# Kernel tuning notes

Measured on AMD Instinct MI355X. Metric: run time of the kernel, lower is better.

## Reference

```python
import jax, jax.numpy as jnp
import numpy as np

# Static config (matches init_kwargs)
VOCAB, EMBED, HIDDEN = 32000, 256, 512
SLOTS, MEM_DIM, HEADS, TOPK = 1024, 64, 4, 8
B, T = 16, 128
# beta_read/beta_write are learned scalars but the torch forward detaches them
# via .item(); treat as constants (|beta| + 1e-6 with beta init ~1.0).
BETA_R = 1.0 + 1e-6
BETA_W = 1.0 + 1e-6
EPS = 1e-8


def setup_inputs() -> dict:
    key = jax.random.key(0)
    ks = jax.random.split(key, 16)
    s = 0.02
    HD = HEADS * MEM_DIM
    return {
        "input_seq": jax.random.randint(ks[0], (B, T), 0, VOCAB),
        "E": jax.random.normal(ks[1], (VOCAB, EMBED), jnp.float32) * s,
        "W_ih": jax.random.normal(ks[2], (4 * HIDDEN, EMBED + MEM_DIM), jnp.float32) * s,
        "W_hh": jax.random.normal(ks[3], (4 * HIDDEN, HIDDEN), jnp.float32) * s,
        "b_ih": jnp.zeros((4 * HIDDEN,), jnp.float32),
        "b_hh": jnp.zeros((4 * HIDDEN,), jnp.float32),
        "W_out": jax.random.normal(ks[4], (HIDDEN, VOCAB), jnp.float32) * s,
        "b_out": jnp.zeros((VOCAB,), jnp.float32),
        "W_rk": jax.random.normal(ks[5], (HIDDEN, HD), jnp.float32) * s,
        "b_rk": jnp.zeros((HD,), jnp.float32),
        "W_wk": jax.random.normal(ks[6], (HIDDEN, HD), jnp.float32) * s,
        "b_wk": jnp.zeros((HD,), jnp.float32),
        "W_wv": jax.random.normal(ks[7], (HIDDEN, HD), jnp.float32) * s,
        "b_wv": jnp.zeros((HD,), jnp.float32),
        "W_er": jax.random.normal(ks[8], (HIDDEN, HD), jnp.float32) * s,
        "b_er": jnp.zeros((HD,), jnp.float32),
    }


def _address(memory, keys, beta):
    # memory: [B,S,D], keys: [B,H,D] -> sparse (top-k) content weights [B,H,S]
    mem_n = memory / (jnp.linalg.norm(memory, axis=-1, keepdims=True) + EPS)
    key_n = keys / (jnp.linalg.norm(keys, axis=-1, keepdims=True) + EPS)
    scores = beta * jnp.einsum("bhd,bsd->bhs", key_n, mem_n)
    vals, idx = jax.lax.top_k(scores, TOPK)           # [B,H,K]
    sm = jax.nn.softmax(vals, axis=-1)                # softmax over top-k only
    w = jnp.zeros_like(scores)
    b_ix = jnp.arange(scores.shape[0])[:, None, None]
    h_ix = jnp.arange(HEADS)[None, :, None]
    return w.at[b_ix, h_ix, idx].set(sm)              # [B,H,S]


def reference(input_seq, E, W_ih, W_hh, b_ih, b_hh, W_out, b_out,
              W_rk, b_rk, W_wk, b_wk, W_wv, b_wv, W_er, b_er):
    Bq = input_seq.shape[0]
    memory0 = jnp.full((Bq, SLOTS, MEM_DIM), 1e-6, jnp.float32)
    h0 = jnp.zeros((Bq, HIDDEN), jnp.float32)
    c0 = jnp.zeros((Bq, HIDDEN), jnp.float32)
    r0 = jnp.zeros((Bq, MEM_DIM), jnp.float32)

    def step(carry, x_t):
        memory, h, c, read_vec = carry
        emb = E[x_t]                                          # [B,embed]
        inp = jnp.concatenate([emb, read_vec], axis=-1)
        gates = inp @ W_ih.T + b_ih + h @ W_hh.T + b_hh       # [B,4H]
        i, f, g, o = jnp.split(gates, 4, axis=-1)             # torch LSTM order
        c = jax.nn.sigmoid(f) * c + jax.nn.sigmoid(i) * jnp.tanh(g)
        h = jax.nn.sigmoid(o) * jnp.tanh(c)
        logits = h @ W_out + b_out                            # [B,V]
        rk = (h @ W_rk + b_rk).reshape(Bq, HEADS, MEM_DIM)
        wk = (h @ W_wk + b_wk).reshape(Bq, HEADS, MEM_DIM)
        wv = (h @ W_wv + b_wv).reshape(Bq, HEADS, MEM_DIM)
        er = jax.nn.sigmoid(h @ W_er + b_er).reshape(Bq, HEADS, MEM_DIM)
        # content-addressed top-k read
        rw = _address(memory, rk, BETA_R)                     # [B,H,S]
        read_vec = jnp.einsum("bhs,bsd->bhd", rw, memory).mean(axis=1)
        # erase + add write
        ww = _address(memory, wk, BETA_W)                     # [B,H,S]
        keep = jnp.prod(1.0 - ww[..., None] * er[:, :, None, :], axis=1)
        add = jnp.einsum("bhs,bhd->bsd", ww, wv)
        memory = memory * keep + add
        return (memory, h, c, read_vec), logits

    _, logits_seq = jax.lax.scan(step, (memory0, h0, c0, r0), input_seq.T)
    return jnp.transpose(logits_seq, (1, 0, 2))               # [B,T,V]
```

## Files before the change

kernel.cpp:

```cpp
#include <hip/hip_runtime.h>
#include <hip/hip_bf16.h>
#include <stdint.h>

typedef unsigned int uint;
typedef unsigned short ushort;
typedef unsigned long long u64;
typedef __attribute__((ext_vector_type(8))) short s8v;
typedef __attribute__((ext_vector_type(4))) float f4v;

#define T_STEPS 128
#define BQ 16
#define HID 512
#define NSLOT 1024
#define MD 64
#define VOCAB 32000
#define BETA 1.000001f
#define EPSN 1e-8f

#define NWK 128
#define NBT 16

#define LF_FH(b)  ((b)*32)
#define LF_FP(w)  ((16+(w))*32)
#define LF_FC(w)  ((48+(w))*32)
#define LF_FRV(b) ((176+(b))*32)
#define LF_FG(w)  ((192+(w))*32)
#define NLINES    320

#define AL4(dst, p) asm volatile("global_load_dwordx4 %0, %1, off sc0 sc1" : "=v"(dst) : "v"(p))
#define ALF(dst, p) asm volatile("global_load_dword %0, %1, off sc0 sc1" : "=v"(dst) : "v"(p))
#define AWAIT() do { asm volatile("s_waitcnt vmcnt(0)" ::: "memory"); __builtin_amdgcn_sched_barrier(0); } while(0)
#define DRAIN() asm volatile("s_waitcnt vmcnt(0)" ::: "memory")

__device__ __forceinline__ float sigm(float x){ return 1.f/(1.f+expf(-x)); }
__device__ __forceinline__ void astoref(float* p, float v){
  __hip_atomic_store(p, v, __ATOMIC_RELAXED, __HIP_MEMORY_SCOPE_AGENT);
}
__device__ __forceinline__ void astoreu32(uint* p, uint v){
  __hip_atomic_store(p, v, __ATOMIC_RELAXED, __HIP_MEMORY_SCOPE_AGENT);
}
__device__ __forceinline__ void astoreu64(u64* p, u64 v){
  __hip_atomic_store(p, v, __ATOMIC_RELAXED, __HIP_MEMORY_SCOPE_AGENT);
}
__device__ __forceinline__ u64 aloadu64(const u64* p){
  return __hip_atomic_load((u64*)p, __ATOMIC_RELAXED, __HIP_MEMORY_SCOPE_AGENT);
}
__device__ __forceinline__ uint aloadu32(const uint* p){
  return __hip_atomic_load((uint*)p, __ATOMIC_RELAXED, __HIP_MEMORY_SCOPE_AGENT);
}
__device__ __forceinline__ void poll1(const uint* p, uint gen){
  while (aloadu32(p) < gen) __builtin_amdgcn_s_sleep(2);
}

__device__ __forceinline__ u64 packsc(float v, int slot){
  uint u = __float_as_uint(v);
  u = (u & 0x80000000u) ? ~u : (u | 0x80000000u);
  return ((u64)u << 10) | (u64)(1023 - slot);
}
__device__ __forceinline__ float unpackval(u64 p){
  uint u = (uint)(p >> 10);
  uint bits = (u & 0x80000000u) ? (u & 0x7fffffffu) : ~u;
  return __uint_as_float(bits);
}
__device__ __forceinline__ int unpackslot(u64 p){ return 1023 - (int)(p & 1023u); }

__device__ __forceinline__ ushort f2bf(float x){
  __hip_bfloat16 h = __float2bfloat16(x);
  return *(ushort*)&h;
}
__device__ __forceinline__ float bf2f(ushort u){
  __hip_bfloat16 h; *(ushort*)&h = u;
  return __bfloat162float(h);
}

#define L_MEM  0
#define L_NRM  8704
#define L_HS   8832
#define L_KEY  17088
#define L_KNRM 17600
#define L_SC   17608
#define L_WV   18632
#define L_ER   18888
#define L_WL   19144
#define L_RVS  19208
#define L_WTS  20232
#define L_TOT  21256

__global__ __launch_bounds__(256) void prep_emb(const float* __restrict__ E,
                                                const int* __restrict__ seq,
                                                float* __restrict__ EMB){
  int m = blockIdx.x, t = m >> 4, b = m & 15;
  int x = seq[b*T_STEPS + t];
  EMB[(size_t)m*256 + threadIdx.x] = E[(size_t)x*256 + threadIdx.x];
}

__global__ __launch_bounds__(256) void gemm_emb(const float* __restrict__ A,
                                                const float* __restrict__ W_ih,
                                                const float* __restrict__ b_ih,
                                                const float* __restrict__ b_hh,
                                                float* __restrict__ C){
  __shared__ __align__(16) float As[16*68];
  __shared__ __align__(16) float Bs[16*68];
  int mt = blockIdx.x & 31, nt = blockIdx.x >> 5;
  int m0 = mt*64, n0 = nt*64;
  int tx = threadIdx.x & 15, ty = threadIdx.x >> 4;
  float acc[4][4] = {};
  for (int k0 = 0; k0 < 256; k0 += 16){
    int mm = threadIdx.x >> 2, kq = (threadIdx.x & 3)*4;
    float4 a = *(const float4*)(A + (size_t)(m0+mm)*256 + k0 + kq);
    As[(kq+0)*68+mm]=a.x; As[(kq+1)*68+mm]=a.y; As[(kq+2)*68+mm]=a.z; As[(kq+3)*68+mm]=a.w;
    int pp = n0 + mm;
    int r = (pp & 3)*512 + (pp >> 2);
    float4 bv = *(const float4*)(W_ih + (size_t)r*320 + k0 + kq);
    Bs[(kq+0)*68+mm]=bv.x; Bs[(kq+1)*68+mm]=bv.y; Bs[(kq+2)*68+mm]=bv.z; Bs[(kq+3)*68+mm]=bv.w;
    __syncthreads();
    #pragma unroll
    for (int kk = 0; kk < 16; ++kk){
      float4 av = *(const float4*)(As + kk*68 + ty*4);
      float4 bb = *(const float4*)(Bs + kk*68 + tx*4);
      float aa[4] = {av.x,av.y,av.z,av.w};
      float bv2[4] = {bb.x,bb.y,bb.z,bb.w};
      #pragma unroll
      for (int i = 0; i < 4; ++i)
        #pragma unroll
        for (int j = 0; j < 4; ++j)
          acc[i][j] = fmaf(aa[i], bv2[j], acc[i][j]);
    }
    __syncthreads();
  }
  #pragma unroll
  for (int i = 0; i < 4; ++i){
    int m = m0 + ty*4 + i;
    #pragma unroll
    for (int j = 0; j < 4; ++j){
      int pp = n0 + tx*4 + j;
      int r = (pp & 3)*512 + (pp >> 2);
      C[(size_t)m*2048 + pp] = acc[i][j] + b_ih[r] + b_hh[r];
    }
  }
}

__global__ __launch_bounds__(256) void make_wrvT(const float* __restrict__ W_ih,
                                                 float* __restrict__ WT){
  int idx = blockIdx.x*256 + threadIdx.x;
  int k = idx >> 11, p = idx & 2047;
  int r = (p & 3)*512 + (p >> 2);
  WT[idx] = W_ih[(size_t)r*320 + 256 + k];
}

__global__ __launch_bounds__(256) void split_BT(const float* __restrict__ W,
                                                ushort* __restrict__ BThi,
                                                ushort* __restrict__ BTlo){
  __shared__ float tl[32][33];
  int kt = blockIdx.x & 15, nt = blockIdx.x >> 4;
  int k0 = kt*32, n0 = nt*32;
  int tx = threadIdx.x & 31, ty = threadIdx.x >> 5;
  #pragma unroll
  for (int i = 0; i < 4; ++i)
    tl[ty + i*8][tx] = W[(size_t)(k0 + ty + i*8)*VOCAB + n0 + tx];
  __syncthreads();
  #pragma unroll
  for (int i = 0; i < 4; ++i){
    float x = tl[tx][ty + i*8];
    ushort hi = f2bf(x);
    ushort lo = f2bf(x - bf2f(hi));
    size_t o = (size_t)(n0 + ty + i*8)*512 + k0 + tx;
    BThi[o] = hi; BTlo[o] = lo;
  }
}

__global__ __launch_bounds__(256) void split_A(const float* __restrict__ H,
                                               ushort* __restrict__ Ahi,
                                               ushort* __restrict__ Alo){
  int idx = blockIdx.x*256 + threadIdx.x;
  float x = H[idx];
  ushort hi = f2bf(x);
  Ahi[idx] = hi;
  Alo[idx] = f2bf(x - bf2f(hi));
}

__global__ __launch_bounds__(256) void recur_kernel(
    const float* __restrict__ W_hh, const float* __restrict__ WT,
    const float* __restrict__ W_rk, const float* __restrict__ b_rk,
    const float* __restrict__ W_wk, const float* __restrict__ b_wk,
    const float* __restrict__ W_wv, const float* __restrict__ b_wv,
    const float* __restrict__ W_er, const float* __restrict__ b_er,
    const float* __restrict__ G_emb, float* __restrict__ H_all,
    float* __restrict__ H_pub, float* __restrict__ mem_g,
    float* __restrict__ projpub, float* __restrict__ gatespub,
    float* __restrict__ rvpub, u64* __restrict__ cand,
    u64* __restrict__ wlist, uint* __restrict__ arrv)
{
  __shared__ __align__(16) float smem[L_TOT];
  const int tid = threadIdx.x;
  const int wg  = blockIdx.x;

  if (wg < NWK){
    float* mem_s  = smem + L_MEM;
    float* nrm_s  = smem + L_NRM;
    float* hs     = smem + L_HS;
    float* key_s  = smem + L_KEY;
    float* knrm_s = smem + L_KNRM;
    float* sc_s   = smem + L_SC;
    float* wv_s   = smem + L_WV;
    float* er_s   = smem + L_ER;
    u64*   wl_s   = (u64*)(smem + L_WL);
    float* rv_s   = smem + L_RVS;
    float* WT_s   = smem + L_WTS;

    const int b_s = wg >> 3, rg = wg & 7, s0 = rg*128;
    const int gb = tid >> 4, gc = tid & 15;
    const int pcol = wg*16 + gc;
    const int rrow = (pcol & 3)*512 + (pcol >> 2);
    float* mslice_g = mem_g + ((size_t)b_s*NSLOT + s0)*MD;
    const float* W1 = (wg < 16) ? W_rk : W_wk;
    const float* B1 = (wg < 16) ? b_rk : b_wk;
    const float* W2 = (wg < 16) ? W_wv : W_er;
    const float* B2 = (wg < 16) ? b_wv : b_er;
    const int cc = (wg & 15)*16 + gc;
    const float pb1 = (wg < 32) ? B1[cc] : 0.f;
    const float pb2 = (wg < 32) ? B2[cc] : 0.f;

    for (int i = tid; i < 64*16; i += 256){
      int d = i >> 4, c = i & 15;
      WT_s[i] = WT[(size_t)d*2048 + wg*16 + c];
    }
    for (int i = tid; i < 128*MD; i += 256){
      mem_s[(i >> 6)*68 + (i & 63)] = 1e-6f;
      astoref(mslice_g + i, 1e-6f);
    }
    __syncthreads();
    {
      int s = tid >> 1, half = tid & 1;
      const float4* mp = (const float4*)(mem_s + s*68 + half*32);
      float sum = 0.f;
      #pragma unroll
      for (int q = 0; q < 8; ++q){
        float4 v = mp[q];
        sum = fmaf(v.x,v.x,sum); sum = fmaf(v.y,v.y,sum);
        sum = fmaf(v.z,v.z,sum); sum = fmaf(v.w,v.w,sum);
      }
      sum += __shfl_xor(sum, 1);
      if (half == 0) nrm_s[s] = sqrtf(sum) + EPSN;
    }
    __syncthreads();

    #pragma clang loop unroll(disable)
    for (int t = 0; t < T_STEPS-1; ++t){
      const int par = t & 1, parp = par ^ 1;
      if (t > 0){
        if (tid < 32) wl_s[tid] = aloadu64(wlist + (size_t)b_s*32 + tid);
        if (tid < 64){
          float4 v; AL4(v, (const float4*)(projpub + (size_t)parp*BQ*1024 + (size_t)b_s*1024 + 512) + tid);
          AWAIT();
          *(float4*)(wv_s + tid*4) = v;
        } else if (tid < 128){
          int i = tid - 64;
          float4 v; AL4(v, (const float4*)(projpub + (size_t)parp*BQ*1024 + (size_t)b_s*1024 + 768) + i);
          AWAIT();
          *(float4*)(er_s + i*4) = v;
        }
        __syncthreads();
        if (tid < 64){
          const int d = tid;
          #pragma unroll 1
          for (int e = 0; e < 32; ++e){
            u64 w64 = wl_s[e];
            int sl = (int)(w64 & 0xffffffffu);
            if (sl >= s0 && sl < s0+128){
              float w = __uint_as_float((uint)(w64 >> 32));
              mem_s[(sl-s0)*68 + d] *= (1.f - w*er_s[(e >> 3)*64 + d]);
            }
          }
          #pragma unroll 1
          for (int e = 0; e < 32; ++e){
            u64 w64 = wl_s[e];
            int sl = (int)(w64 & 0xffffffffu);
            if (sl >= s0 && sl < s0+128){
              float w = __uint_as_float((uint)(w64 >> 32));
              mem_s[(sl-s0)*68 + d] += w*wv_s[(e >> 3)*64 + d];
            }
          }
          #pragma unroll 1
          for (int e = 0; e < 32; ++e){
            u64 w64 = wl_s[e];
            int sl = (int)(w64 & 0xffffffffu);
            if (sl >= s0 && sl < s0+128)
              astoref(mslice_g + (sl-s0)*MD + d, mem_s[(sl-s0)*68 + d]);
          }
        }
        __syncthreads();
        {
          int s = tid >> 1, half = tid & 1;
          const float4* mp = (const float4*)(mem_s + s*68 + half*32);
          float sum = 0.f;
          #pragma unroll
          for (int q = 0; q < 8; ++q){
            float4 v = mp[q];
            sum = fmaf(v.x,v.x,sum); sum = fmaf(v.y,v.y,sum);
            sum = fmaf(v.z,v.z,sum); sum = fmaf(v.w,v.w,sum);
          }
          sum += __shfl_xor(sum, 1);
          if (half == 0) nrm_s[s] = sqrtf(sum) + EPSN;
        }
      }
      if (tid < 16) poll1(arrv + LF_FH(tid), (uint)(t+1));
      __syncthreads();
      {
        float4 v0,v1,v2,v3,v4,v5,v6,v7;
        const float4* hp = (const float4*)H_pub;
        AL4(v0, hp + tid);        AL4(v1, hp + tid + 256);
        AL4(v2, hp + tid + 512);  AL4(v3, hp + tid + 768);
        AL4(v4, hp + tid + 1024); AL4(v5, hp + tid + 1280);
        AL4(v6, hp + tid + 1536); AL4(v7, hp + tid + 1792);
        AWAIT();
        int i;
        i = tid;        *(float4*)(hs + (i>>7)*516 + (i&127)*4) = v0;
        i = tid + 256;  *(float4*)(hs + (i>>7)*516 + (i&127)*4) = v1;
        i = tid + 512;  *(float4*)(hs + (i>>7)*516 + (i&127)*4) = v2;
        i = tid + 768;  *(float4*)(hs + (i>>7)*516 + (i&127)*4) = v3;
        i = tid + 1024; *(float4*)(hs + (i>>7)*516 + (i&127)*4) = v4;
        i = tid + 1280; *(float4*)(hs + (i>>7)*516 + (i&127)*4) = v5;
        i = tid + 1536; *(float4*)(hs + (i>>7)*516 + (i&127)*4) = v6;
        i = tid + 1792; *(float4*)(hs + (i>>7)*516 + (i&127)*4) = v7;
      }
      __syncthreads();
      if (wg < 32){
        float a0=0.f,a1=0.f,b0=0.f,b1=0.f;
        const float* hp = hs + gb*516;
        const float* w1 = W1 + cc;
        const float* w2 = W2 + cc;
        #pragma unroll 4
        for (int k = 0; k < 512; k += 2){
          float h0 = hp[k], h1 = hp[k+1];
          a0 = fmaf(h0, w1[(size_t)k*256], a0);
          b0 = fmaf(h0, w2[(size_t)k*256], b0);
          a1 = fmaf(h1, w1[(size_t)(k+1)*256], a1);
          b1 = fmaf(h1, w2[(size_t)(k+1)*256], b1);
        }
        float v1 = a0 + a1 + pb1;
        float v2 = b0 + b1 + pb2;
        if (wg >= 16) v2 = sigm(v2);
        astoref(projpub + (size_t)par*BQ*1024 + (size_t)gb*1024 + wg*16 + gc, v1);
        astoref(projpub + (size_t)par*BQ*1024 + (size_t)gb*1024 + 512 + wg*16 + gc, v2);
      }
      DRAIN();
      __syncthreads();
      if (wg < 32 && tid == 0) astoreu32(arrv + LF_FP(wg), (uint)(t+1));
      if (tid < 32) poll1(arrv + LF_FP(tid), (uint)(t+1));
      __syncthreads();
      if (tid < 128){
        float4 kv; AL4(kv, (const float4*)(projpub + (size_t)par*BQ*1024 + (size_t)b_s*1024) + tid);
        AWAIT();
        *(float4*)(key_s + tid*4) = kv;
      }
      __syncthreads();
      if (tid < 8){
        const float4* kp = (const float4*)(key_s + tid*MD);
        float sum = 0.f;
        #pragma unroll
        for (int q = 0; q < 16; ++q){
          float4 v = kp[q];
          sum = fmaf(v.x,v.x,sum); sum = fmaf(v.y,v.y,sum);
          sum = fmaf(v.z,v.z,sum); sum = fmaf(v.w,v.w,sum);
        }
        knrm_s[tid] = sqrtf(sum) + EPSN;
      }
      __syncthreads();
      {
        int s = tid >> 1, kh = tid & 1;
        const float4* mp = (const float4*)(mem_s + s*68);
        float rnm = 1.f / nrm_s[s];
        float acc4[4] = {0.f,0.f,0.f,0.f};
        #pragma unroll
        for (int q = 0; q < 16; ++q){
          float4 m = mp[q];
          #pragma unroll
          for (int kk = 0; kk < 4; ++kk){
            float4 k4 = *(const float4*)(key_s + (kh*4+kk)*MD + q*4);
            acc4[kk] = fmaf(m.x,k4.x,acc4[kk]); acc4[kk] = fmaf(m.y,k4.y,acc4[kk]);
            acc4[kk] = fmaf(m.z,k4.z,acc4[kk]); acc4[kk] = fmaf(m.w,k4.w,acc4[kk]);
          }
        }
        #pragma unroll
        for (int kk = 0; kk < 4; ++kk){
          int key = kh*4 + kk;
          sc_s[key*128 + s] = BETA * acc4[kk] * rnm / knrm_s[key];
        }
      }
      __syncthreads();
      {
        int wid = tid >> 6, lane = tid & 63;
        #pragma unroll
        for (int kk = 0; kk < 2; ++kk){
          int key = wid*2 + kk;
          u64 p0 = packsc(sc_s[key*128 + lane],      s0 + lane);
          u64 p1 = packsc(sc_s[key*128 + 64 + lane], s0 + 64 + lane);
          #pragma unroll
          for (int r = 0; r < 8; ++r){
            u64 m = p0 > p1 ? p0 : p1;
            #pragma unroll
            for (int o = 32; o; o >>= 1){ u64 q = __shfl_xor(m, o); if (q > m) m = q; }
            if (p0 == m) p0 = 0; else if (p1 == m) p1 = 0;
            if (lane == 0) astoreu64(cand + (((size_t)b_s*8 + key)*8 + rg)*8 + r, m);
          }
        }
      }
      DRAIN();
      __syncthreads();
      if (tid == 0) astoreu32(arrv + LF_FC(wg), (uint)(t+1));
      float gpv;
      {
        float a0 = G_emb[(size_t)((t+1)*BQ + gb)*2048 + pcol];
        float a1 = 0.f, a2 = 0.f, a3 = 0.f;
        const float4* wh = (const float4*)(W_hh + (size_t)rrow*HID);
        const float4* xv = (const float4*)(hs + gb*516);
        #pragma unroll 2
        for (int k = 0; k < 128; k += 4){
          float4 w, x;
          w=wh[k+0]; x=xv[k+0]; a0=fmaf(w.x,x.x,a0); a0=fmaf(w.y,x.y,a0); a0=fmaf(w.z,x.z,a0); a0=fmaf(w.w,x.w,a0);
          w=wh[k+1]; x=xv[k+1]; a1=fmaf(w.x,x.x,a1); a1=fmaf(w.y,x.y,a1); a1=fmaf(w.z,x.z,a1); a1=fmaf(w.w,x.w,a1);
          w=wh[k+2]; x=xv[k+2]; a2=fmaf(w.x,x.x,a2); a2=fmaf(w.y,x.y,a2); a2=fmaf(w.z,x.z,a2); a2=fmaf(w.w,x.w,a2);
          w=wh[k+3]; x=xv[k+3]; a3=fmaf(w.x,x.x,a3); a3=fmaf(w.y,x.y,a3); a3=fmaf(w.z,x.z,a3); a3=fmaf(w.w,x.w,a3);
        }
        gpv = (a0+a1)+(a2+a3);
      }
      if (tid < 16) poll1(arrv + LF_FRV(tid), (uint)(t+1));
      __syncthreads();
      {
        float4 v; AL4(v, (const float4*)rvpub + tid); AWAIT();
        *(float4*)(rv_s + tid*4) = v;
      }
      __syncthreads();
      {
        float acc = gpv;
        #pragma unroll 8
        for (int d = 0; d < 64; ++d)
          acc = fmaf(rv_s[gb*64 + d], WT_s[d*16 + gc], acc);
        astoref(gatespub + (size_t)gb*2048 + pcol, acc);
      }
      DRAIN();
      __syncthreads();
      if (tid == 0) astoreu32(arrv + LF_FG(wg), (uint)(t+1));
    }
  } else {
    const int b = wg - NWK;
    float* rv_st = smem;
    float c0, c1;
    {
      float4 gA = *(const float4*)(G_emb + (size_t)b*2048 + tid*8);
      float4 gB = *(const float4*)(G_emb + (size_t)b*2048 + tid*8 + 4);
      c0 = sigm(gA.x)*tanhf(gA.z);
      float h0v = sigm(gA.w)*tanhf(c0);
      c1 = sigm(gB.x)*tanhf(gB.z);
      float h1v = sigm(gB.w)*tanhf(c1);
      astoref(H_pub + (size_t)b*HID + tid*2,     h0v);
      astoref(H_pub + (size_t)b*HID + tid*2 + 1, h1v);
      H_all[(size_t)b*HID + tid*2]     = h0v;
      H_all[(size_t)b*HID + tid*2 + 1] = h1v;
    }
    DRAIN();
    __syncthreads();
    if (tid == 0) astoreu32(arrv + LF_FH(b), 1u);

    #pragma clang loop unroll(disable)
    for (int t = 0; t < T_STEPS-1; ++t){
      if (tid < 8) poll1(arrv + LF_FC(b*8 + tid), (uint)(t+1));
      __syncthreads();
      {
        int wid = tid >> 6, lane = tid & 63;
        #pragma unroll
        for (int kk = 0; kk < 2; ++kk){
          int key = wid*2 + kk;
          u64 pv = aloadu64(cand + (((size_t)b*8 + key)*8 + (lane >> 3))*8 + (lane & 7));
          u64 sel = 0;
          #pragma unroll
          for (int r = 0; r < 8; ++r){
            u64 m = pv;
            #pragma unroll
            for (int o = 32; o; o >>= 1){ u64 q = __shfl_xor(m, o); if (q > m) m = q; }
            if (pv == m) pv = 0;
            if (lane == r) sel = m;
          }
          float val = unpackval(sel);
          int slot = unpackslot(sel);
          float vmax = __shfl(val, 0);
          float e = (lane < 8) ? expf(val - vmax) : 0.f;
          float ssum = e;
          #pragma unroll
          for (int o = 32; o; o >>= 1) ssum += __shfl_xor(ssum, o);
          float w = e / ssum;
          if (key < 4){
            int sls[8];
            #pragma unroll
            for (int i = 0; i < 8; ++i) sls[i] = __shfl(slot, i);
            float mv[8];
            #pragma unroll
            for (int i = 0; i < 8; ++i)
              ALF(mv[i], mem_g + ((size_t)b*NSLOT + sls[i])*MD + lane);
            AWAIT();
            float acc = 0.f;
            #pragma unroll
            for (int i = 0; i < 8; ++i) acc = fmaf(__shfl(w, i), mv[i], acc);
            rv_st[key*64 + lane] = acc;
          } else if (lane < 8){
            astoreu64(wlist + (size_t)b*32 + (key-4)*8 + lane,
                      ((u64)__float_as_uint(w) << 32) | (u64)(uint)slot);
          }
        }
      }
      __syncthreads();
      if (tid < 64){
        float m = 0.25f*(rv_st[tid] + rv_st[64+tid] + rv_st[128+tid] + rv_st[192+tid]);
        astoref(rvpub + (size_t)b*MD + tid, m);
      }
      DRAIN();
      __syncthreads();
      if (tid == 0) astoreu32(arrv + LF_FRV(b), (uint)(t+1));
      if (tid < 128) poll1(arrv + LF_FG(tid), (uint)(t+1));
      __syncthreads();
      {
        float4 gA, gB;
        AL4(gA, (const float4*)(gatespub + (size_t)b*2048) + tid*2);
        AL4(gB, (const float4*)(gatespub + (size_t)b*2048) + tid*2 + 1);
        AWAIT();
        c0 = sigm(gA.y)*c0 + sigm(gA.x)*tanhf(gA.z);
        float h0v = sigm(gA.w)*tanhf(c0);
        c1 = sigm(gB.y)*c1 + sigm(gB.x)*tanhf(gB.z);
        float h1v = sigm(gB.w)*tanhf(c1);
        astoref(H_pub + (size_t)b*HID + tid*2,     h0v);
        astoref(H_pub + (size_t)b*HID + tid*2 + 1, h1v);
        H_all[(size_t)((t+1)*BQ + b)*HID + tid*2]     = h0v;
        H_all[(size_t)((t+1)*BQ + b)*HID + tid*2 + 1] = h1v;
      }
      DRAIN();
      __syncthreads();
      if (tid == 0) astoreu32(arrv + LF_FH(b), (uint)(t+2));
    }
  }
}

#define GM_NT 250
__global__ __launch_bounds__(256) void gemm_mfma(
    const ushort* __restrict__ Ahi, const ushort* __restrict__ Alo,
    const ushort* __restrict__ BThi, const ushort* __restrict__ BTlo,
    const float* __restrict__ bias, float* __restrict__ C)
{
  __shared__ __align__(16) ushort ldsu[4*128*40];
  const int tid = threadIdx.x;
  int mt = blockIdx.x / GM_NT, nt = blockIdx.x - mt*GM_NT;
  int m0 = mt*128, n0 = nt*128;
  const int wv = tid >> 6, lane = tid & 63;
  const int wm = (wv & 1)*64, wn = (wv >> 1)*64;
  const int fr = lane & 15, kh = (lane >> 4)*8;

  f4v acc[4][4];
  #pragma unroll
  for (int i = 0; i < 4; ++i)
    #pragma unroll
    for (int j = 0; j < 4; ++j)
      acc[i][j] = (f4v){0.f,0.f,0.f,0.f};

  const int sr = tid & 127, sel = tid >> 7;
  const ushort* srcA = (sel ? Alo : Ahi) + (size_t)(m0 + sr)*512;
  const ushort* srcB = (sel ? BTlo : BThi) + (size_t)(n0 + sr)*512;
  ushort* dstA = ldsu + (size_t)sel*5120 + sr*40;
  ushort* dstB = ldsu + (size_t)(2+sel)*5120 + sr*40;

  for (int ks = 0; ks < 16; ++ks){
    const int k0 = ks*32;
    __syncthreads();
    {
      uint4 a0 = *(const uint4*)(srcA + k0);
      uint4 a1 = *(const uint4*)(srcA + k0 + 8);
      uint4 a2 = *(const uint4*)(srcA + k0 + 16);
      uint4 a3 = *(const uint4*)(srcA + k0 + 24);
      uint4 b0 = *(const uint4*)(srcB + k0);
      uint4 b1 = *(const uint4*)(srcB + k0 + 8);
      uint4 b2 = *(const uint4*)(srcB + k0 + 16);
      uint4 b3 = *(const uint4*)(srcB + k0 + 24);
      *(uint4*)(dstA +  0) = a0; *(uint4*)(dstA +  8) = a1;
      *(uint4*)(dstA + 16) = a2; *(uint4*)(dstA + 24) = a3;
      *(uint4*)(dstB +  0) = b0; *(uint4*)(dstB +  8) = b1;
      *(uint4*)(dstB + 16) = b2; *(uint4*)(dstB + 24) = b3;
    }
    __syncthreads();
    s8v ah[4], al[4], bh[4], bl[4];
    #pragma unroll
    for (int mi = 0; mi < 4; ++mi){
      ah[mi] = *(const s8v*)(ldsu + 0*5120 + (wm + mi*16 + fr)*40 + kh);
      al[mi] = *(const s8v*)(ldsu + 1*5120 + (wm + mi*16 + fr)*40 + kh);
    }
    #pragma unroll
    for (int ni = 0; ni < 4; ++ni){
      bh[ni] = *(const s8v*)(ldsu + 2*5120 + (wn + ni*16 + fr)*40 + kh);
      bl[ni] = *(const s8v*)(ldsu + 3*5120 + (wn + ni*16 + fr)*40 + kh);
    }
    #pragma unroll
    for (int mi = 0; mi < 4; ++mi)
      #pragma unroll
      for (int ni = 0; ni < 4; ++ni){
        acc[mi][ni] = __builtin_amdgcn_mfma_f32_16x16x32_bf16(ah[mi], bh[ni], acc[mi][ni], 0, 0, 0);
        acc[mi][ni] = __builtin_amdgcn_mfma_f32_16x16x32_bf16(ah[mi], bl[ni], acc[mi][ni], 0, 0, 0);
        acc[mi][ni] = __builtin_amdgcn_mfma_f32_16x16x32_bf16(al[mi], bh[ni], acc[mi][ni], 0, 0, 0);
        acc[mi][ni] = __builtin_amdgcn_mfma_f32_16x16x32_bf16(al[mi], bl[ni], acc[mi][ni], 0, 0, 0);
      }
  }
  #pragma unroll
  for (int ni = 0; ni < 4; ++ni){
    int col = n0 + wn + ni*16 + fr;
    float bz = bias[col];
    #pragma unroll
    for (int mi = 0; mi < 4; ++mi){
      #pragma unroll
      for (int j = 0; j < 4; ++j){
        int row = m0 + wm + mi*16 + (lane >> 4)*4 + j;
        C[((size_t)(row & 15)*T_STEPS + (row >> 4))*VOCAB + col] = acc[mi][ni][j] + bz;
      }
    }
  }
}

__global__ __launch_bounds__(256) void gemm_out(const float* __restrict__ A,
                                                const float* __restrict__ Bmat,
                                                const float* __restrict__ bias,
                                                float* __restrict__ C){
  __shared__ __align__(16) float As[16*132];
  __shared__ __align__(16) float Bs[16*64];
  int mt = blockIdx.x & 15, nt = blockIdx.x >> 4;
  int m0 = mt*128, n0 = nt*64;
  int tx = threadIdx.x & 15, ty = threadIdx.x >> 4;
  float acc[8][4] = {};
  for (int k0 = 0; k0 < 512; k0 += 16){
    int mm = threadIdx.x >> 1, kq = (threadIdx.x & 1)*8;
    float4 a0 = *(const float4*)(A + (size_t)(m0+mm)*512 + k0 + kq);
    float4 a1 = *(const float4*)(A + (size_t)(m0+mm)*512 + k0 + kq + 4);
    As[(kq+0)*132+mm]=a0.x; As[(kq+1)*132+mm]=a0.y; As[(kq+2)*132+mm]=a0.z; As[(kq+3)*132+mm]=a0.w;
    As[(kq+4)*132+mm]=a1.x; As[(kq+5)*132+mm]=a1.y; As[(kq+6)*132+mm]=a1.z; As[(kq+7)*132+mm]=a1.w;
    int kk2 = threadIdx.x >> 4, nq = (threadIdx.x & 15)*4;
    *(float4*)(Bs + kk2*64 + nq) = *(const float4*)(Bmat + (size_t)(k0+kk2)*VOCAB + n0 + nq);
    __syncthreads();
    #pragma unroll
    for (int kk = 0; kk < 16; ++kk){
      float4 x0 = *(const float4*)(As + kk*132 + ty*8);
      float4 x1 = *(const float4*)(As + kk*132 + ty*8 + 4);
      float4 bv = *(const float4*)(Bs + kk*64 + tx*4);
      float aa[8] = {x0.x,x0.y,x0.z,x0.w,x1.x,x1.y,x1.z,x1.w};
      float bb[4] = {bv.x,bv.y,bv.z,bv.w};
      #pragma unroll
      for (int i = 0; i < 8; ++i)
        #pragma unroll
        for (int j = 0; j < 4; ++j)
          acc[i][j] = fmaf(aa[i], bb[j], acc[i][j]);
    }
    __syncthreads();
  }
  #pragma unroll
  for (int i = 0; i < 8; ++i){
    int m = m0 + ty*8 + i;
    int bq = m & 15, tt = m >> 4;
    float* crow = C + ((size_t)bq*T_STEPS + tt)*VOCAB + n0 + tx*4;
    #pragma unroll
    for (int j = 0; j < 4; ++j) crow[j] = acc[i][j] + bias[n0 + tx*4 + j];
  }
}

extern "C" void kernel_launch(void* const* d_in, const int* in_sizes, int n_in,
                              void* d_out, int out_size, void* d_ws, size_t ws_size,
                              hipStream_t stream){
  const int*   seq   = (const int*)d_in[0];
  const float* E     = (const float*)d_in[1];
  const float* W_ih  = (const float*)d_in[2];
  const float* W_hh  = (const float*)d_in[3];
  const float* b_ih  = (const float*)d_in[4];
  const float* b_hh  = (const float*)d_in[5];
  const float* W_out = (const float*)d_in[6];
  const float* b_out = (const float*)d_in[7];
  const float* W_rk  = (const float*)d_in[8];
  const float* b_rk  = (const float*)d_in[9];
  const float* W_wk  = (const float*)d_in[10];
  const float* b_wk  = (const float*)d_in[11];
  const float* W_wv  = (const float*)d_in[12];
  const float* b_wv  = (const float*)d_in[13];
  const float* W_er  = (const float*)d_in[14];
  const float* b_er  = (const float*)d_in[15];
  float* out = (float*)d_out;
  (void)in_sizes; (void)n_in; (void)out_size;

  char* ws = (char*)d_ws;
  size_t off = 0;
  auto alloc = [&](size_t bytes) -> void* {
    off = (off + 255) & ~(size_t)255;
    void* p = ws + off;
    off += bytes;
    return p;
  };
  float* EMB      = (float*)alloc((size_t)2048*256*4);
  float* G_emb    = (float*)alloc((size_t)2048*2048*4);
  float* H_all    = (float*)alloc((size_t)2048*512*4);
  float* H_pub    = (float*)alloc((size_t)16*512*4);
  float* mem_g    = (float*)alloc((size_t)16*1024*64*4);
  float* projpub  = (float*)alloc((size_t)2*16*1024*4);
  float* gatespub = (float*)alloc((size_t)16*2048*4);
  float* rvpub    = (float*)alloc((size_t)16*64*4);
  u64*   cand     = (u64*)alloc((size_t)16*8*8*8*8);
  u64*   wlist    = (u64*)alloc((size_t)16*32*8);
  float* WT       = (float*)alloc((size_t)64*2048*4);
  uint*  arrv     = (uint*)alloc((size_t)NLINES*32*4);
  ushort* Ahi  = (ushort*)alloc((size_t)2048*512*2);
  ushort* Alo  = (ushort*)alloc((size_t)2048*512*2);
  ushort* BThi = (ushort*)alloc((size_t)VOCAB*512*2);
  ushort* BTlo = (ushort*)alloc((size_t)VOCAB*512*2);
  const bool use_mfma = (off <= ws_size);

  hipMemsetAsync(arrv, 0, (size_t)NLINES*32*4, stream);
  prep_emb<<<2048, 256, 0, stream>>>(E, seq, EMB);
  gemm_emb<<<1024, 256, 0, stream>>>(EMB, W_ih, b_ih, b_hh, G_emb);
  make_wrvT<<<512, 256, 0, stream>>>(W_ih, WT);
  if (use_mfma)
    split_BT<<<16000, 256, 0, stream>>>(W_out, BThi, BTlo);
  recur_kernel<<<NWK + NBT, 256, 0, stream>>>(
      W_hh, WT, W_rk, b_rk, W_wk, b_wk, W_wv, b_wv, W_er, b_er,
      G_emb, H_all, H_pub, mem_g, projpub, gatespub, rvpub, cand, wlist, arrv);
  if (use_mfma){
    split_A<<<4096, 256, 0, stream>>>(H_all, Ahi, Alo);
    gemm_mfma<<<16*GM_NT, 256, 0, stream>>>(Ahi, Alo, BThi, BTlo, b_out, out);
  } else {
    gemm_out<<<16*500, 256, 0, stream>>>(H_all, W_out, b_out, out);
  }
}
```

Before: 6.497 ms.

## Move read-vector gate contribution into per-batch LSTM blocks, drop rv publish handshake

The read-vector term (rv @ W_ih[:,emb:]) is now computed by each per-batch LSTM workgroup directly from WT in global memory, after loading the recurrent gate partials. Worker workgroups no longer wait for rvpub from all batches before publishing gates, which removes one cross-workgroup barrier from the per-step critical path. In exchange, each batch block does a 64x2048 matvec reading WT from global or L2 every step, and workers now poll a new write-list flag before reading wlist.

```diff
diff --git a/kernel.cpp b/kernel.cpp
--- a/kernel.cpp
+++ b/kernel.cpp
@@ -23,7 +23,7 @@
 #define LF_FH(b)  ((b)*32)
 #define LF_FP(w)  ((16+(w))*32)
 #define LF_FC(w)  ((48+(w))*32)
-#define LF_FRV(b) ((176+(b))*32)
+#define LF_FW(b)  ((176+(b))*32)
 #define LF_FG(w)  ((192+(w))*32)
 #define NLINES    320
 
@@ -82,9 +82,7 @@
 #define L_WV   18632
 #define L_ER   18888
 #define L_WL   19144
-#define L_RVS  19208
-#define L_WTS  20232
-#define L_TOT  21256
+#define L_TOT  19208
 
 __global__ __launch_bounds__(256) void prep_emb(const float* __restrict__ E,
                                                 const int* __restrict__ seq,
@@ -188,8 +186,8 @@
     const float* __restrict__ G_emb, float* __restrict__ H_all,
     float* __restrict__ H_pub, float* __restrict__ mem_g,
     float* __restrict__ projpub, float* __restrict__ gatespub,
-    float* __restrict__ rvpub, u64* __restrict__ cand,
-    u64* __restrict__ wlist, uint* __restrict__ arrv)
+    u64* __restrict__ cand, u64* __restrict__ wlist,
+    uint* __restrict__ arrv)
 {
   __shared__ __align__(16) float smem[L_TOT];
   const int tid = threadIdx.x;
@@ -205,8 +203,6 @@
     float* wv_s   = smem + L_WV;
     float* er_s   = smem + L_ER;
     u64*   wl_s   = (u64*)(smem + L_WL);
-    float* rv_s   = smem + L_RVS;
-    float* WT_s   = smem + L_WTS;
 
     const int b_s = wg >> 3, rg = wg & 7, s0 = rg*128;
     const int gb = tid >> 4, gc = tid & 15;
@@ -221,10 +217,6 @@
     const float pb1 = (wg < 32) ? B1[cc] : 0.f;
     const float pb2 = (wg < 32) ? B2[cc] : 0.f;
 
-    for (int i = tid; i < 64*16; i += 256){
-      int d = i >> 4, c = i & 15;
-      WT_s[i] = WT[(size_t)d*2048 + wg*16 + c];
-    }
     for (int i = tid; i < 128*MD; i += 256){
       mem_s[(i >> 6)*68 + (i & 63)] = 1e-6f;
       astoref(mslice_g + i, 1e-6f);
@@ -249,6 +241,8 @@
     for (int t = 0; t < T_STEPS-1; ++t){
       const int par = t & 1, parp = par ^ 1;
       if (t > 0){
+        if (tid == 0) poll1(arrv + LF_FW(b_s), (uint)t);
+        __syncthreads();
         if (tid < 32) wl_s[tid] = aloadu64(wlist + (size_t)b_s*32 + tid);
         if (tid < 64){
           float4 v; AL4(v, (const float4*)(projpub + (size_t)parp*BQ*1024 + (size_t)b_s*1024 + 512) + tid);
@@ -409,7 +403,6 @@
       DRAIN();
       __syncthreads();
       if (tid == 0) astoreu32(arrv + LF_FC(wg), (uint)(t+1));
-      float gpv;
       {
         float a0 = G_emb[(size_t)((t+1)*BQ + gb)*2048 + pcol];
         float a1 = 0.f, a2 = 0.f, a3 = 0.f;
@@ -423,21 +416,7 @@
           w=wh[k+2]; x=xv[k+2]; a2=fmaf(w.x,x.x,a2); a2=fmaf(w.y,x.y,a2); a2=fmaf(w.z,x.z,a2); a2=fmaf(w.w,x.w,a2);
           w=wh[k+3]; x=xv[k+3]; a3=fmaf(w.x,x.x,a3); a3=fmaf(w.y,x.y,a3); a3=fmaf(w.z,x.z,a3); a3=fmaf(w.w,x.w,a3);
         }
-        gpv = (a0+a1)+(a2+a3);
-      }
-      if (tid < 16) poll1(arrv + LF_FRV(tid), (uint)(t+1));
-      __syncthreads();
-      {
-        float4 v; AL4(v, (const float4*)rvpub + tid); AWAIT();
-        *(float4*)(rv_s + tid*4) = v;
-      }
-      __syncthreads();
-      {
-        float acc = gpv;
-        #pragma unroll 8
-        for (int d = 0; d < 64; ++d)
-          acc = fmaf(rv_s[gb*64 + d], WT_s[d*16 + gc], acc);
-        astoref(gatespub + (size_t)gb*2048 + pcol, acc);
+        astoref(gatespub + (size_t)gb*2048 + pcol, (a0+a1)+(a2+a3));
       }
       DRAIN();
       __syncthreads();
@@ -446,6 +425,8 @@
   } else {
     const int b = wg - NWK;
     float* rv_st = smem;
+    float* rv_s  = smem + 256;
+    float* gl    = smem + 320;
     float c0, c1;
     {
       float4 gA = *(const float4*)(G_emb + (size_t)b*2048 + tid*8);
@@ -509,25 +490,38 @@
           }
         }
       }
-      __syncthreads();
-      if (tid < 64){
-        float m = 0.25f*(rv_st[tid] + rv_st[64+tid] + rv_st[128+tid] + rv_st[192+tid]);
-        astoref(rvpub + (size_t)b*MD + tid, m);
-      }
       DRAIN();
       __syncthreads();
-      if (tid == 0) astoreu32(arrv + LF_FRV(b), (uint)(t+1));
+      if (tid < 64)
+        rv_s[tid] = 0.25f*(rv_st[tid] + rv_st[64+tid] + rv_st[128+tid] + rv_st[192+tid]);
+      if (tid == 0) astoreu32(arrv + LF_FW(b), (uint)(t+1));
       if (tid < 128) poll1(arrv + LF_FG(tid), (uint)(t+1));
       __syncthreads();
       {
-        float4 gA, gB;
-        AL4(gA, (const float4*)(gatespub + (size_t)b*2048) + tid*2);
-        AL4(gB, (const float4*)(gatespub + (size_t)b*2048) + tid*2 + 1);
+        float g8[8];
+        #pragma unroll
+        for (int q = 0; q < 8; ++q)
+          ALF(g8[q], gatespub + (size_t)b*2048 + tid + 256*q);
         AWAIT();
-        c0 = sigm(gA.y)*c0 + sigm(gA.x)*tanhf(gA.z);
-        float h0v = sigm(gA.w)*tanhf(c0);
-        c1 = sigm(gB.y)*c1 + sigm(gB.x)*tanhf(gB.z);
-        float h1v = sigm(gB.w)*tanhf(c1);
+        #pragma unroll 2
+        for (int d = 0; d < 64; ++d){
+          float r = rv_s[d];
+          const float* wrow = WT + (size_t)d*2048 + tid;
+          #pragma unroll
+          for (int q = 0; q < 8; ++q)
+            g8[q] = fmaf(r, wrow[256*q], g8[q]);
+        }
+        #pragma unroll
+        for (int q = 0; q < 8; ++q) gl[tid + 256*q] = g8[q];
+      }
+      __syncthreads();
+      {
+        float gi0 = gl[tid*8+0], gf0 = gl[tid*8+1], gg0 = gl[tid*8+2], go0 = gl[tid*8+3];
+        float gi1 = gl[tid*8+4], gf1 = gl[tid*8+5], gg1 = gl[tid*8+6], go1 = gl[tid*8+7];
+        c0 = sigm(gf0)*c0 + sigm(gi0)*tanhf(gg0);
+        float h0v = sigm(go0)*tanhf(c0);
+        c1 = sigm(gf1)*c1 + sigm(gi1)*tanhf(gg1);
+        float h1v = sigm(go1)*tanhf(c1);
         astoref(H_pub + (size_t)b*HID + tid*2,     h0v);
         astoref(H_pub + (size_t)b*HID + tid*2 + 1, h1v);
         H_all[(size_t)((t+1)*BQ + b)*HID + tid*2]     = h0v;
@@ -702,7 +696,6 @@
   float* mem_g    = (float*)alloc((size_t)16*1024*64*4);
   float* projpub  = (float*)alloc((size_t)2*16*1024*4);
   float* gatespub = (float*)alloc((size_t)16*2048*4);
-  float* rvpub    = (float*)alloc((size_t)16*64*4);
   u64*   cand     = (u64*)alloc((size_t)16*8*8*8*8);
   u64*   wlist    = (u64*)alloc((size_t)16*32*8);
   float* WT       = (float*)alloc((size_t)64*2048*4);
@@ -721,7 +714,7 @@
     split_BT<<<16000, 256, 0, stream>>>(W_out, BThi, BTlo);
   recur_kernel<<<NWK + NBT, 256, 0, stream>>>(
       W_hh, WT, W_rk, b_rk, W_wk, b_wk, W_wv, b_wv, W_er, b_er,
-      G_emb, H_all, H_pub, mem_g, projpub, gatespub, rvpub, cand, wlist, arrv);
+      G_emb, H_all, H_pub, mem_g, projpub, gatespub, cand, wlist, arrv);
   if (use_mfma){
     split_A<<<4096, 256, 0, stream>>>(H_all, Ahi, Alo);
     gemm_mfma<<<16*GM_NT, 256, 0, stream>>>(Ahi, Alo, BThi, BTlo, b_out, out);
```

Measured after the change: 6.386 ms, median of 2. Within noise of the previous version (-1.7%).
